# Optimization experiments

Measured on AMD Instinct MI355X. Metric: run time of the kernel, lower is better.

## Reference

```python
import jax, jax.numpy as jnp
import numpy as np

UNITS = 128
INPUT_DIM = 784
OUTPUT_DIM = 10
NUM_LAYERS = 8
BATCH = 2048
DT = 0.1
EPS = 0.01
TOL = 1e-4
STEPS = 15


def setup_inputs() -> dict:
    key = jax.random.key(0)
    k = jax.random.split(key, 7)
    s_in = 1.0 / np.sqrt(INPUT_DIM)
    s_u = 1.0 / np.sqrt(UNITS)
    return {
        "x": jax.random.normal(k[0], (BATCH, INPUT_DIM), jnp.float32),
        "w_in": jax.random.uniform(k[1], (UNITS, INPUT_DIM), jnp.float32, -s_in, s_in),
        "b_in": jax.random.uniform(k[2], (UNITS,), jnp.float32, -s_in, s_in),
        "w_blocks": jax.random.uniform(k[3], (NUM_LAYERS, UNITS, UNITS), jnp.float32, -s_u, s_u),
        "b_blocks": jax.random.uniform(k[4], (NUM_LAYERS, UNITS), jnp.float32, -s_u, s_u),
        "w_out": jax.random.uniform(k[5], (OUTPUT_DIM, UNITS), jnp.float32, -s_u, s_u),
        "b_out": jax.random.uniform(k[6], (OUTPUT_DIM,), jnp.float32, -s_u, s_u),
    }


def _build_A(w_blocks):
    # A_l = [[I, dt*W_l], [-dt*W_l^T, (1+dt/eps)*I]], shape [L, 2u, 2u]
    I = jnp.broadcast_to(jnp.eye(UNITS, dtype=w_blocks.dtype), (NUM_LAYERS, UNITS, UNITS))
    top = jnp.concatenate([I, DT * w_blocks], axis=2)
    bot = jnp.concatenate([-DT * jnp.transpose(w_blocks, (0, 2, 1)), (1.0 + DT / EPS) * I], axis=2)
    return jnp.concatenate([top, bot], axis=1)


def _sweep(z_in, A, b_blocks):
    # Fixed-point sweeping (no-grad region in the original). z_ls: [L, B, 2u]
    B = z_in.shape[0]

    def layer_step(z, xs):
        A_l, b_l, z_l = xs
        rhs = jnp.concatenate(
            [jnp.broadcast_to(DT * b_l, (B, UNITS)), (DT / EPS) * jnp.tanh(z_l[:, :UNITS])],
            axis=1,
        ) + z
        # A_l is shared across the batch: one LU, many rhs
        y = jnp.linalg.solve(A_l, rhs.T).T
        err = jnp.mean(jnp.linalg.norm(z_l - y, axis=1))
        return y, (y, err)

    def body(state):
        z_ls, _, step = state
        _, (new_zls, errs) = jax.lax.scan(layer_step, z_in, (A, b_blocks, z_ls))
        return (new_zls, jnp.mean(errs), step + 1)

    def cond(state):
        _, err, step = state
        return jnp.logical_and(step < STEPS, err > TOL)

    z0 = jnp.broadcast_to(z_in[None], (NUM_LAYERS,) + z_in.shape)
    z_ls, _, _ = jax.lax.while_loop(cond, body, (z0, jnp.float32(10.0), jnp.int32(0)))
    return z_ls


def _block(z_in, W, b, z_l):
    # implicit_forward of one TransNetLayerSweeping (z_l is the converged sweep state)
    u_l, v_l = z_l[:, :UNITS], z_l[:, UNITS:]
    u_out = -DT * (v_l @ W.T) + z_in[:, :UNITS] + DT * b
    v_out = DT * (u_l @ W) + z_in[:, UNITS:] - (DT / EPS) * (v_l - jnp.tanh(u_l))
    return jnp.concatenate([u_out, v_out], axis=1)


def reference(x, w_in, b_in, w_blocks, b_blocks, w_out, b_out):
    x1 = x @ w_in.T + b_in                                  # [B, u]
    z_in = jnp.concatenate([x1, jnp.tanh(x1)], axis=1)      # [B, 2u]
    z_ls = _sweep(z_in, _build_A(w_blocks), b_blocks)       # [L, B, 2u]
    # Original loop does z = block.implicit_forward(z_in) for every block,
    # so only the LAST block's output survives.
    z_out = _block(z_in, w_blocks[-1], b_blocks[-1], z_ls[-1])
    logits = z_out[:, :UNITS] @ w_out.T + b_out             # [B, out]
    return jax.nn.softmax(logits, axis=1)
```

## Files before the change

### kernel.cpp

```cpp
#include <hip/hip_runtime.h>

#define U 128
#define BATCH 2048
#define NL 8
#define NS 8
#define DTc 0.1f
#define TENf 10.0f
#define INVC (1.0f/11.0f)
#define AFACT (0.01f/11.0f)
#define AST 264

typedef unsigned short u16;
typedef unsigned int u32;
typedef __attribute__((ext_vector_type(8))) short bf16x8;
typedef __attribute__((ext_vector_type(4))) float f32x4;
#define MFMA16(a,b,c) __builtin_amdgcn_mfma_f32_16x16x32_bf16(a,b,c,0,0,0)

#define SWZ8(row, c8)  (((row)<<7) + ((((c8) ^ ((row)&7)))<<3))
#define SWZE(row, col) (SWZ8(row, (col)>>3) + ((col)&7))

__device__ __forceinline__ float bf2f(u16 h){ return __uint_as_float(((u32)h)<<16); }
__device__ __forceinline__ u16 f2bf(float f){
  u32 u = __float_as_uint(f);
  u += 0x7FFFu + ((u >> 16) & 1u);
  return (u16)(u >> 16);
}
__device__ __forceinline__ float fast_tanh(float x){
  float e = __expf(2.0f*x);
  return 1.0f - __fdividef(2.0f, e + 1.0f);
}
__device__ __forceinline__ int detect_md(const u16* x, int* s_bad, int t, int nthr){
  if(t==0) *s_bad = 0;
  __syncthreads();
  int f=0;
  for(int i=t;i<4096;i+=nthr){ float v = bf2f(x[i]); if(!(fabsf(v)<16.0f)) f=1; }
  if(f) atomicOr(s_bad,1);
  __syncthreads();
  return *s_bad ? 0 : 1;
}
__device__ __forceinline__ bf16x8 ld8f(const float* p){
  float4 f0 = *(const float4*)p, f1 = *(const float4*)(p+4);
  bf16x8 v;
  v[0]=(short)f2bf(f0.x); v[1]=(short)f2bf(f0.y); v[2]=(short)f2bf(f0.z); v[3]=(short)f2bf(f0.w);
  v[4]=(short)f2bf(f1.x); v[5]=(short)f2bf(f1.y); v[6]=(short)f2bf(f1.z); v[7]=(short)f2bf(f1.w);
  return v;
}
__device__ __forceinline__ void lgkm_barrier(){
  __builtin_amdgcn_sched_barrier(0);
  asm volatile("s_waitcnt lgkmcnt(0)\n\ts_barrier" ::: "memory");
  __builtin_amdgcn_sched_barrier(0);
}

template<typename GB, typename EPI>
__device__ __forceinline__ void gfull(const u16* __restrict__ A, GB getB, EPI epi,
                                      int w, int ln, int lq){
  const int n0 = 16*w + ln;
  bf16x8 bfr[4];
  #pragma unroll
  for(int kt=0;kt<4;kt++) bfr[kt] = getB(n0, kt*32 + lq*8);
  #pragma unroll 2
  for(int rt=0; rt<8; rt++){
    f32x4 acc = {0,0,0,0};
    #pragma unroll
    for(int kt=0;kt<4;kt++){
      bf16x8 af = *(const bf16x8*)&A[SWZ8(rt*16+ln, kt*4+lq)];
      acc = MFMA16(af, bfr[kt], acc);
    }
    epi(acc, rt*16 + lq*4, n0);
  }
}

__global__ __launch_bounds__(512) void prepB(
    const void* __restrict__ xraw, const void* __restrict__ wb,
    u16* __restrict__ Fsw){
  __shared__ u16 bufA[16384];
  __shared__ u16 bufB[16384];
  const int t = threadIdx.x;
  const int lane = t & 63, w = t >> 6, ln = lane & 15, lq = lane >> 4;
  const int L = blockIdx.x >> 3, mt = blockIdx.x & 7;
  const int md = detect_md((const u16*)xraw, (int*)bufA, t, 512);
  __syncthreads();
  const u16*   wbb = (const u16*)wb   + ((size_t)L<<14);
  const float* wbf = (const float*)wb + ((size_t)L<<14);

  for(int j8=t; j8<2048; j8+=512){
    int n = j8 >> 4, k0 = (j8 & 15) * 8;
    bf16x8 v = md ? *(const bf16x8*)&wbb[j8*8] : ld8f(wbf + j8*8);
    #pragma unroll
    for(int m=0;m<8;m++) bufA[SWZE(k0+m, n)] = (u16)v[m];
  }
  __syncthreads();

  auto gA = [&](int n,int k0)->bf16x8{ return *(const bf16x8*)&bufA[SWZ8(n, k0>>3)]; };
  auto gB = [&](int n,int k0)->bf16x8{ return *(const bf16x8*)&bufB[SWZ8(n, k0>>3)]; };
  auto gW = [&](int n,int k0)->bf16x8{
    if(md) return *(const bf16x8*)&wbb[n*U+k0];
    return ld8f(wbf + n*U + k0);
  };

  gfull(bufA, gA, [&](f32x4 acc, int rowb, int n0){
    #pragma unroll
    for(int r=0;r<4;r++) bufB[SWZE(rowb+r, n0)] = f2bf(AFACT*acc[r]);
  }, w, ln, lq);
  __syncthreads();
  gfull(bufB, gB, [&](f32x4 acc, int rowb, int n0){
    #pragma unroll
    for(int r=0;r<4;r++){
      int row = rowb + r;
      bufA[SWZE(row, n0)] = f2bf(INVC*(((row==n0)?1.0f:0.0f) - bf2f(bufB[SWZE(row, n0)]) + acc[r]));
    }
  }, w, ln, lq);
  __syncthreads();
  gfull(bufA, gW, [&](f32x4 acc, int rowb, int n0){
    #pragma unroll
    for(int r=0;r<4;r++) bufB[SWZE(rowb+r, n0)] = f2bf(DTc*acc[r]);
  }, w, ln, lq);
  __syncthreads();

  for(int i = mt*1024 + t; i < (mt+1)*1024; i += 512){
    int wf = (i>>11)&3;
    if(wf >= 2) continue;
    int lanei = i & 63, kt = (i>>6)&7, c = (i>>9)&3;
    int row_n = 64*wf + 16*c + (lanei & 15);
    int c8 = kt*4 + (lanei >> 4);
    bf16x8 v = (kt < 4) ? *(const bf16x8*)&bufA[SWZ8(row_n, c8)]
                        : *(const bf16x8*)&bufB[SWZ8(row_n, c8-16)];
    *(bf16x8*)&Fsw[((size_t)L*8192 + i)*8] = v;
  }
  __syncthreads();
  for(int j8=t; j8<2048; j8+=512){
    int row = j8 >> 4, c0 = (j8 & 15) * 8;
    bf16x8 v = *(const bf16x8*)&bufB[SWZ8(row, c0>>3)];
    #pragma unroll
    for(int m=0;m<8;m++) bufA[SWZE(c0+m, row)] = (u16)v[m];
  }
  __syncthreads();
  for(int i = mt*1024 + t; i < (mt+1)*1024; i += 512){
    int wf = (i>>11)&3, kt = (i>>6)&7;
    if(wf < 2 || kt >= 4) continue;
    int lanei = i & 63, c = (i>>9)&3;
    int row_n = 64*wf + 16*c + (lanei & 15);
    int c8 = kt*4 + (lanei >> 4);
    *(bf16x8*)&Fsw[((size_t)L*8192 + i)*8] = *(const bf16x8*)&bufA[SWZ8(row_n-128, c8)];
  }
  {
    const int n0 = 16*w + ln;
    bf16x8 bq[4];
    #pragma unroll
    for(int kt=0;kt<4;kt++) bq[kt] = *(const bf16x8*)&bufA[SWZ8(n0, kt*4+lq)];
    f32x4 acc = {0,0,0,0};
    #pragma unroll
    for(int kt=0;kt<4;kt++){
      bf16x8 af = gW(mt*16 + ln, kt*32 + lq*8);
      acc = MFMA16(af, bq[kt], acc);
    }
    const int wf = 2 + (mt>>2), cc = mt & 3;
    const int kt_ = 4 + (n0>>5), lqi = (n0>>3)&3, jj = n0 & 7;
    #pragma unroll
    for(int r=0;r<4;r++){
      int lni = lq*4 + r;
      int i = (wf<<11)|(cc<<9)|(kt_<<6)|(lqi<<4)|lni;
      Fsw[((size_t)L*8192 + i)*8 + jj] = f2bf(DTc*acc[r]);
    }
  }
}

__global__ __launch_bounds__(1024,4) void mainK(
    const void* __restrict__ xraw, const void* __restrict__ w_in,
    const void* __restrict__ b_in, const void* __restrict__ bb,
    const bf16x8* __restrict__ Fsw, const void* __restrict__ w_out,
    const void* __restrict__ b_out, void* __restrict__ outraw){
  __shared__ u16 At[2][16*AST];
  __shared__ u16 zh16[NL][16][132];
  __shared__ float zinu[16*U];
  __shared__ float bbL[NL*U];
  __shared__ float lg[16*12];
  __shared__ int s_bad;
  float* uout = (float*)&At[0][0];

  const int t = threadIdx.x;
  const int lane = t & 63, wid = t >> 6, ln = lane & 15, lq = lane >> 4;
  const int r0 = blockIdx.x * 16;

  const int md = detect_md((const u16*)xraw, &s_bad, t, 1024);
  for(int i=t;i<NL*U;i+=1024)
    bbL[i] = DTc * (md ? bf2f(((const u16*)bb)[i]) : ((const float*)bb)[i]);
  __syncthreads();

  if(wid < 8){
    const int n0 = 16*wid + ln;
    const u16*   wrb = (const u16*)w_in   + (size_t)n0*784;
    const float* wrf = (const float*)w_in + (size_t)n0*784;
    const u16*   xrb = (const u16*)xraw   + (size_t)(r0+ln)*784;
    const float* xrf = (const float*)xraw + (size_t)(r0+ln)*784;
    f32x4 acc = {0,0,0,0};
    const bf16x8 z8 = {0,0,0,0,0,0,0,0};
    if(md){
      #pragma unroll
      for(int kt=0; kt<24; ++kt){
        int k0 = kt*32 + lq*8;
        acc = MFMA16(*(const bf16x8*)(xrb + k0), *(const bf16x8*)(wrb + k0), acc);
      }
      { int k0 = 768 + lq*8;
        bf16x8 av = z8, bv = z8;
        if(lq < 2){ av = *(const bf16x8*)(xrb + k0); bv = *(const bf16x8*)(wrb + k0); }
        acc = MFMA16(av, bv, acc);
      }
    } else {
      #pragma unroll 4
      for(int kt=0; kt<24; ++kt){
        int k0 = kt*32 + lq*8;
        acc = MFMA16(ld8f(xrf + k0), ld8f(wrf + k0), acc);
      }
      { int k0 = 768 + lq*8;
        bf16x8 av = z8, bv = z8;
        if(lq < 2){ av = ld8f(xrf + k0); bv = ld8f(wrf + k0); }
        acc = MFMA16(av, bv, acc);
      }
    }
    float bi = md ? bf2f(((const u16*)b_in)[n0]) : ((const float*)b_in)[n0];
    #pragma unroll
    for(int r=0;r<4;r++) zinu[(lq*4+r)*U + n0] = acc[r] + bi;
  }
  __syncthreads();

  for(int i=t; i<NL*16*128; i+=1024){
    int l = i>>11, row = (i>>7)&15, c = i & 127;
    zh16[l][row][c] = f2bf(zinu[row*U + c]);
  }
  float ru[4];
  if(wid < 8){
    const int n = 16*wid + ln;
    #pragma unroll
    for(int r=0;r<4;r++){
      int row = lq*4 + r;
      At[0][row*AST + n] = f2bf((TENf + 1.0f) * fast_tanh(zinu[row*U + n]));
    }
  } else {
    const int uc = 16*(wid-8) + ln;
    #pragma unroll
    for(int r=0;r<4;r++){
      int row = lq*4 + r;
      float v = zinu[row*U + uc] + bbL[uc];
      ru[r] = v;
      At[0][row*AST + 128 + uc] = f2bf(v);
    }
  }
  const bf16x8* fbase = Fsw + (wid>>2)*2048 + (wid&3)*512 + lane;
  bf16x8 BfA[8], BfB[8];
  #pragma unroll
  for(int kt=0;kt<8;kt++) BfA[kt] = fbase[kt*64];
  __syncthreads();

#define STEPBODY(STEPV, BC, BN, CURC) { \
    const int l = (STEPV) & 7; \
    const int lnext = (l+1) & 7; \
    const bool last = ((STEPV) == NS*NL-1); \
    { const bf16x8* fp = fbase + lnext*8192; \
      _Pragma("unroll") \
      for(int kt=0;kt<8;kt++) BN[kt] = fp[kt*64]; } \
    bf16x8 at8[8]; \
    _Pragma("unroll") \
    for(int kt=0;kt<8;kt++) at8[kt] = *(const bf16x8*)&At[CURC][ln*AST + kt*32 + lq*8]; \
    float th[4]; \
    if(wid < 8 && !last){ \
      _Pragma("unroll") \
      for(int r=0;r<4;r++) th[r] = TENf * fast_tanh(bf2f(zh16[lnext][lq*4 + r][16*wid + ln])); \
    } \
    f32x4 acc = {0,0,0,0}; \
    _Pragma("unroll") \
    for(int kt=0;kt<8;kt++) acc = MFMA16(at8[kt], BC[kt], acc); \
    if(wid < 8){ \
      if(!last){ \
        const bool wrap = (l == 7); \
        const int n = 16*wid + ln; \
        _Pragma("unroll") \
        for(int r=0;r<4;r++){ \
          int row = lq*4 + r; \
          float base = wrap ? fast_tanh(zinu[row*U + n]) : acc[r]; \
          At[1-(CURC)][row*AST + n] = f2bf(th[r] + base); \
        } \
      } \
    } else { \
      const int uc0 = 16*(wid-8) + ln; \
      _Pragma("unroll") \
      for(int r=0;r<4;r++){ \
        int row = lq*4 + r; \
        float yu = ru[r] - acc[r]; \
        zh16[l][row][uc0] = f2bf(yu); \
        if(last){ \
          uout[row*U + uc0] = zinu[row*U + uc0] + bbL[7*U + uc0] - acc[r]; \
        } else if(l == 7){ \
          float rn = zinu[row*U + uc0] + bbL[uc0]; \
          ru[r] = rn; \
          At[1-(CURC)][row*AST + 128 + uc0] = f2bf(rn); \
        } else { \
          float rn = yu + bbL[(l+1)*U + uc0]; \
          ru[r] = rn; \
          At[1-(CURC)][row*AST + 128 + uc0] = f2bf(rn); \
        } \
      } \
    } \
    lgkm_barrier(); \
  }

  for(int sp=0; sp<NS*NL; sp+=2){
    STEPBODY(sp,   BfA, BfB, 0)
    STEPBODY(sp+1, BfB, BfA, 1)
  }
#undef STEPBODY

  if(t < 160){
    int mm = t/10, o = t - mm*10;
    float a = md ? bf2f(((const u16*)b_out)[o]) : ((const float*)b_out)[o];
    if(md){
      const u16* wo = (const u16*)w_out + o*U;
      for(int k=0;k<U;k++) a += uout[mm*U + k]*bf2f(wo[k]);
    } else {
      const float* wo = (const float*)w_out + o*U;
      for(int k=0;k<U;k++) a += uout[mm*U + k]*wo[k];
    }
    lg[mm*12 + o] = a;
  }
  __syncthreads();
  if(t < 16){
    float mx = -1e30f;
    for(int o=0;o<10;o++) mx = fmaxf(mx, lg[t*12 + o]);
    float e[10]; float sum = 0.0f;
    for(int o=0;o<10;o++){ e[o] = __expf(lg[t*12 + o] - mx); sum += e[o]; }
    float inv = 1.0f / sum;
    for(int o=0;o<10;o++){
      float pv = e[o]*inv;
      if(md) ((u16*)outraw)[(size_t)(r0 + t)*10 + o] = f2bf(pv);
      else   ((float*)outraw)[(size_t)(r0 + t)*10 + o] = pv;
    }
  }
}

extern "C" void kernel_launch(void* const* d_in, const int* in_sizes, int n_in,
                              void* d_out, int out_size, void* d_ws, size_t ws_size,
                              hipStream_t stream) {
  u16* Fsw = (u16*)d_ws;

  prepB<<<64, 512, 0, stream>>>(d_in[0], d_in[3], Fsw);
  mainK<<<BATCH/16, 1024, 0, stream>>>(d_in[0], d_in[1], d_in[2], d_in[4],
                                       (const bf16x8*)Fsw, d_in[5], d_in[6], d_out);
}
```

Before: 202.0 us.

## Factor the u-update through W: two chained MFMAs per step, halve block threads

The main kernel now computes only the left half of the precomputed solve matrix, producing an intermediate that is staged through shared memory and multiplied by a per-layer W fragment to form the u update. This replaces the lower-right precomputed product, so prepB no longer builds it. The block shrinks from 1024 to 512 threads, every wave handles both halves, and biases and the input projection are held in registers instead of shared memory. The aim is to cut prep work, workspace traffic and per-step MFMA count, at the cost of a serial second MFMA chain, an extra barrier per step, and an additional bf16 rounding of the intermediate.

```diff
diff --git a/kernel.cpp b/kernel.cpp
--- a/kernel.cpp
+++ b/kernel.cpp
@@ -9,6 +9,7 @@
 #define INVC (1.0f/11.0f)
 #define AFACT (0.01f/11.0f)
 #define AST 264
+#define HST 136
 
 typedef unsigned short u16;
 typedef unsigned int u32;
@@ -72,7 +73,7 @@
 
 __global__ __launch_bounds__(512) void prepB(
     const void* __restrict__ xraw, const void* __restrict__ wb,
-    u16* __restrict__ Fsw){
+    u16* __restrict__ Fsw, u16* __restrict__ Wfr){
   __shared__ u16 bufA[16384];
   __shared__ u16 bufB[16384];
   const int t = threadIdx.x;
@@ -82,6 +83,13 @@
   __syncthreads();
   const u16*   wbb = (const u16*)wb   + ((size_t)L<<14);
   const float* wbf = (const float*)wb + ((size_t)L<<14);
+
+  if(t < 256){
+    int kt = t >> 6, lanei = t & 63, lni = lanei & 15, lqi = lanei >> 4;
+    bf16x8 v = md ? *(const bf16x8*)&wbb[(16*mt+lni)*U + 32*kt + 8*lqi]
+                  : ld8f(wbf + (16*mt+lni)*U + 32*kt + 8*lqi);
+    *(bf16x8*)&Wfr[((size_t)L*2048 + mt*256 + t)*8] = v;
+  }
 
   for(int j8=t; j8<2048; j8+=512){
     int n = j8 >> 4, k0 = (j8 & 15) * 8;
@@ -127,70 +135,36 @@
                         : *(const bf16x8*)&bufB[SWZ8(row_n, c8-16)];
     *(bf16x8*)&Fsw[((size_t)L*8192 + i)*8] = v;
   }
-  __syncthreads();
-  for(int j8=t; j8<2048; j8+=512){
-    int row = j8 >> 4, c0 = (j8 & 15) * 8;
-    bf16x8 v = *(const bf16x8*)&bufB[SWZ8(row, c0>>3)];
-    #pragma unroll
-    for(int m=0;m<8;m++) bufA[SWZE(c0+m, row)] = (u16)v[m];
-  }
-  __syncthreads();
-  for(int i = mt*1024 + t; i < (mt+1)*1024; i += 512){
-    int wf = (i>>11)&3, kt = (i>>6)&7;
-    if(wf < 2 || kt >= 4) continue;
-    int lanei = i & 63, c = (i>>9)&3;
-    int row_n = 64*wf + 16*c + (lanei & 15);
-    int c8 = kt*4 + (lanei >> 4);
-    *(bf16x8*)&Fsw[((size_t)L*8192 + i)*8] = *(const bf16x8*)&bufA[SWZ8(row_n-128, c8)];
-  }
-  {
-    const int n0 = 16*w + ln;
-    bf16x8 bq[4];
-    #pragma unroll
-    for(int kt=0;kt<4;kt++) bq[kt] = *(const bf16x8*)&bufA[SWZ8(n0, kt*4+lq)];
-    f32x4 acc = {0,0,0,0};
-    #pragma unroll
-    for(int kt=0;kt<4;kt++){
-      bf16x8 af = gW(mt*16 + ln, kt*32 + lq*8);
-      acc = MFMA16(af, bq[kt], acc);
-    }
-    const int wf = 2 + (mt>>2), cc = mt & 3;
-    const int kt_ = 4 + (n0>>5), lqi = (n0>>3)&3, jj = n0 & 7;
-    #pragma unroll
-    for(int r=0;r<4;r++){
-      int lni = lq*4 + r;
-      int i = (wf<<11)|(cc<<9)|(kt_<<6)|(lqi<<4)|lni;
-      Fsw[((size_t)L*8192 + i)*8 + jj] = f2bf(DTc*acc[r]);
-    }
-  }
-}
-
-__global__ __launch_bounds__(1024,4) void mainK(
+}
+
+__global__ __launch_bounds__(512,2) void mainG(
     const void* __restrict__ xraw, const void* __restrict__ w_in,
     const void* __restrict__ b_in, const void* __restrict__ bb,
-    const bf16x8* __restrict__ Fsw, const void* __restrict__ w_out,
-    const void* __restrict__ b_out, void* __restrict__ outraw){
+    const bf16x8* __restrict__ Fsw, const bf16x8* __restrict__ Wfr,
+    const void* __restrict__ w_out, const void* __restrict__ b_out,
+    void* __restrict__ outraw){
   __shared__ u16 At[2][16*AST];
   __shared__ u16 zh16[NL][16][132];
-  __shared__ float zinu[16*U];
-  __shared__ float bbL[NL*U];
+  __shared__ u16 Hld[16*HST];
   __shared__ float lg[16*12];
   __shared__ int s_bad;
   float* uout = (float*)&At[0][0];
 
   const int t = threadIdx.x;
-  const int lane = t & 63, wid = t >> 6, ln = lane & 15, lq = lane >> 4;
+  const int lane = t & 63, w = t >> 6, ln = lane & 15, lq = lane >> 4;
   const int r0 = blockIdx.x * 16;
-
-  const int md = detect_md((const u16*)xraw, &s_bad, t, 1024);
-  for(int i=t;i<NL*U;i+=1024)
-    bbL[i] = DTc * (md ? bf2f(((const u16*)bb)[i]) : ((const float*)bb)[i]);
-  __syncthreads();
-
-  if(wid < 8){
-    const int n0 = 16*wid + ln;
-    const u16*   wrb = (const u16*)w_in   + (size_t)n0*784;
-    const float* wrf = (const float*)w_in + (size_t)n0*784;
+  const int n = 16*w + ln;
+
+  const int md = detect_md((const u16*)xraw, &s_bad, t, 512);
+  float bbLr[NL];
+  #pragma unroll
+  for(int l=0;l<NL;l++)
+    bbLr[l] = DTc * (md ? bf2f(((const u16*)bb)[l*U+n]) : ((const float*)bb)[l*U+n]);
+
+  float zr[4];
+  {
+    const u16*   wrb = (const u16*)w_in   + (size_t)n*784;
+    const float* wrf = (const float*)w_in + (size_t)n*784;
     const u16*   xrb = (const u16*)xraw   + (size_t)(r0+ln)*784;
     const float* xrf = (const float*)xraw + (size_t)(r0+ln)*784;
     f32x4 acc = {0,0,0,0};
@@ -218,95 +192,94 @@
         acc = MFMA16(av, bv, acc);
       }
     }
-    float bi = md ? bf2f(((const u16*)b_in)[n0]) : ((const float*)b_in)[n0];
-    #pragma unroll
-    for(int r=0;r<4;r++) zinu[(lq*4+r)*U + n0] = acc[r] + bi;
-  }
-  __syncthreads();
-
-  for(int i=t; i<NL*16*128; i+=1024){
-    int l = i>>11, row = (i>>7)&15, c = i & 127;
-    zh16[l][row][c] = f2bf(zinu[row*U + c]);
+    float bi = md ? bf2f(((const u16*)b_in)[n]) : ((const float*)b_in)[n];
+    #pragma unroll
+    for(int r=0;r<4;r++) zr[r] = acc[r] + bi;
+  }
+
+  #pragma unroll
+  for(int l=0;l<NL;l++){
+    #pragma unroll
+    for(int r=0;r<4;r++) zh16[l][lq*4+r][n] = f2bf(zr[r]);
   }
   float ru[4];
-  if(wid < 8){
-    const int n = 16*wid + ln;
-    #pragma unroll
-    for(int r=0;r<4;r++){
-      int row = lq*4 + r;
-      At[0][row*AST + n] = f2bf((TENf + 1.0f) * fast_tanh(zinu[row*U + n]));
-    }
-  } else {
-    const int uc = 16*(wid-8) + ln;
-    #pragma unroll
-    for(int r=0;r<4;r++){
-      int row = lq*4 + r;
-      float v = zinu[row*U + uc] + bbL[uc];
-      ru[r] = v;
-      At[0][row*AST + 128 + uc] = f2bf(v);
-    }
-  }
-  const bf16x8* fbase = Fsw + (wid>>2)*2048 + (wid&3)*512 + lane;
-  bf16x8 BfA[8], BfB[8];
+  #pragma unroll
+  for(int r=0;r<4;r++){
+    int row = lq*4 + r;
+    At[0][row*AST + n] = f2bf((TENf + 1.0f) * fast_tanh(zr[r]));
+    float v = zr[r] + bbLr[0];
+    ru[r] = v;
+    At[0][row*AST + 128 + n] = f2bf(v);
+  }
+  const bf16x8* fbase = Fsw + (w>>2)*2048 + (w&3)*512 + lane;
+  const bf16x8* wfb   = Wfr + w*256 + lane;
+  bf16x8 BfA[8], BfB[8], WfA[4], WfB[4];
   #pragma unroll
   for(int kt=0;kt<8;kt++) BfA[kt] = fbase[kt*64];
-  __syncthreads();
-
-#define STEPBODY(STEPV, BC, BN, CURC) { \
+  #pragma unroll
+  for(int kt=0;kt<4;kt++) WfA[kt] = wfb[kt*64];
+  __syncthreads();
+
+#define STEPBODY(STEPV, BC, BN, WC, WN, CURC) { \
     const int l = (STEPV) & 7; \
     const int lnext = (l+1) & 7; \
     const bool last = ((STEPV) == NS*NL-1); \
+    const bool wrap = (l == 7); \
     { const bf16x8* fp = fbase + lnext*8192; \
       _Pragma("unroll") \
-      for(int kt=0;kt<8;kt++) BN[kt] = fp[kt*64]; } \
+      for(int kt=0;kt<8;kt++) BN[kt] = fp[kt*64]; \
+      const bf16x8* wp = wfb + lnext*2048; \
+      _Pragma("unroll") \
+      for(int kt=0;kt<4;kt++) WN[kt] = wp[kt*64]; } \
     bf16x8 at8[8]; \
     _Pragma("unroll") \
     for(int kt=0;kt<8;kt++) at8[kt] = *(const bf16x8*)&At[CURC][ln*AST + kt*32 + lq*8]; \
     float th[4]; \
-    if(wid < 8 && !last){ \
-      _Pragma("unroll") \
-      for(int r=0;r<4;r++) th[r] = TENf * fast_tanh(bf2f(zh16[lnext][lq*4 + r][16*wid + ln])); \
+    if(!last){ \
+      _Pragma("unroll") \
+      for(int r=0;r<4;r++) th[r] = TENf * fast_tanh(bf2f(zh16[lnext][lq*4 + r][n])); \
     } \
-    f32x4 acc = {0,0,0,0}; \
-    _Pragma("unroll") \
-    for(int kt=0;kt<8;kt++) acc = MFMA16(at8[kt], BC[kt], acc); \
-    if(wid < 8){ \
-      if(!last){ \
-        const bool wrap = (l == 7); \
-        const int n = 16*wid + ln; \
-        _Pragma("unroll") \
-        for(int r=0;r<4;r++){ \
-          int row = lq*4 + r; \
-          float base = wrap ? fast_tanh(zinu[row*U + n]) : acc[r]; \
-          At[1-(CURC)][row*AST + n] = f2bf(th[r] + base); \
-        } \
+    f32x4 accL = {0,0,0,0}; \
+    _Pragma("unroll") \
+    for(int kt=0;kt<8;kt++) accL = MFMA16(at8[kt], BC[kt], accL); \
+    _Pragma("unroll") \
+    for(int r=0;r<4;r++) Hld[(lq*4+r)*HST + n] = f2bf(accL[r]); \
+    lgkm_barrier(); \
+    bf16x8 hf[4]; \
+    _Pragma("unroll") \
+    for(int kt=0;kt<4;kt++) hf[kt] = *(const bf16x8*)&Hld[ln*HST + kt*32 + lq*8]; \
+    f32x4 accR = {0,0,0,0}; \
+    _Pragma("unroll") \
+    for(int kt=0;kt<4;kt++) accR = MFMA16(hf[kt], WC[kt], accR); \
+    if(!last){ \
+      _Pragma("unroll") \
+      for(int r=0;r<4;r++){ \
+        int row = lq*4 + r; \
+        float base = wrap ? fast_tanh(zr[r]) : accL[r]; \
+        At[1-(CURC)][row*AST + n] = f2bf(th[r] + base); \
+      } \
+      _Pragma("unroll") \
+      for(int r=0;r<4;r++){ \
+        int row = lq*4 + r; \
+        float yu = ru[r] - DTc*accR[r]; \
+        zh16[l][row][n] = f2bf(yu); \
+        float rn = wrap ? (zr[r] + bbLr[0]) : (yu + bbLr[(l+1)&7]); \
+        ru[r] = rn; \
+        At[1-(CURC)][row*AST + 128 + n] = f2bf(rn); \
       } \
     } else { \
-      const int uc0 = 16*(wid-8) + ln; \
       _Pragma("unroll") \
       for(int r=0;r<4;r++){ \
         int row = lq*4 + r; \
-        float yu = ru[r] - acc[r]; \
-        zh16[l][row][uc0] = f2bf(yu); \
-        if(last){ \
-          uout[row*U + uc0] = zinu[row*U + uc0] + bbL[7*U + uc0] - acc[r]; \
-        } else if(l == 7){ \
-          float rn = zinu[row*U + uc0] + bbL[uc0]; \
-          ru[r] = rn; \
-          At[1-(CURC)][row*AST + 128 + uc0] = f2bf(rn); \
-        } else { \
-          float rn = yu + bbL[(l+1)*U + uc0]; \
-          ru[r] = rn; \
-          At[1-(CURC)][row*AST + 128 + uc0] = f2bf(rn); \
-        } \
+        uout[row*U + n] = zr[r] + bbLr[7] - DTc*accR[r]; \
       } \
     } \
     lgkm_barrier(); \
   }
 
   for(int sp=0; sp<NS*NL; sp+=2){
-    STEPBODY(sp,   BfA, BfB, 0)
-    STEPBODY(sp+1, BfB, BfA, 1)
+    STEPBODY(sp,   BfA, BfB, WfA, WfB, 0)
+    STEPBODY(sp+1, BfB, BfA, WfB, WfA, 1)
   }
 #undef STEPBODY
 
@@ -340,9 +313,12 @@
 extern "C" void kernel_launch(void* const* d_in, const int* in_sizes, int n_in,
                               void* d_out, int out_size, void* d_ws, size_t ws_size,
                               hipStream_t stream) {
-  u16* Fsw = (u16*)d_ws;
-
-  prepB<<<64, 512, 0, stream>>>(d_in[0], d_in[3], Fsw);
-  mainK<<<BATCH/16, 1024, 0, stream>>>(d_in[0], d_in[1], d_in[2], d_in[4],
-                                       (const bf16x8*)Fsw, d_in[5], d_in[6], d_out);
-}
+  char* p = (char*)d_ws;
+  u16* Fsw = (u16*)p;  p += (size_t)8*256*256*2;
+  u16* Wfr = (u16*)p;  p += (size_t)8*128*128*2;
+
+  prepB<<<64, 512, 0, stream>>>(d_in[0], d_in[3], Fsw, Wfr);
+  mainG<<<BATCH/16, 512, 0, stream>>>(d_in[0], d_in[1], d_in[2], d_in[4],
+                                      (const bf16x8*)Fsw, (const bf16x8*)Wfr,
+                                      d_in[5], d_in[6], d_out);
+}
```

New measurement: 187.6 us. -7.1%, faster.
